# Optimization experiments

Measured on AMD Instinct MI355X. Metric: run time of the kernel, lower is better.

## Reference

```python
import jax, jax.numpy as jnp
import numpy as np

N = 1048576  # batch elements; each element is a 64-bit FP64 value stored as {0,1} float bits


def _xor(a, b):
    return a + b - 2.0 * a * b


def _mux(s, a, b):
    # s ? a : b  (spiking MUX gate)
    return s * a + (1.0 - s) * b


def _ripple_add(a, b, c0):
    """Bitwise ripple-carry add of little-endian bit vectors a,b [..., n] with carry-in c0 [...]."""
    def step(carry, ab):
        ai, bi = ab
        x = _xor(ai, bi)
        s = _xor(x, carry)
        c = ai * bi + carry * x - ai * bi * carry * x  # OR(a&b, c&(a^b))
        return c, s
    _, sums = jax.lax.scan(step, c0, (jnp.moveaxis(a, -1, 0), jnp.moveaxis(b, -1, 0)))
    return jnp.moveaxis(sums, 0, -1)


def setup_inputs() -> dict:
    key = jax.random.key(0)
    kx, kk = jax.random.split(key)
    x = jax.random.randint(kx, (N, 64), 0, 2).astype(jnp.float32)
    k = jax.random.randint(kk, (N, 64), 0, 2).astype(jnp.float32)
    return {"x": x, "k": k}


def reference(x, k):
    batch = x.shape[:-1]
    dt = x.dtype
    ones = jnp.ones(batch, dt)
    zeros = jnp.zeros(batch, dt)

    s_x = x[..., 0:1]
    e_x = x[..., 1:12]
    m_x = x[..., 12:64]
    s_k = k[..., 0:1]
    e_k = k[..., 1:12]
    m_k = k[..., 12:64]

    # shift = e_k - 1023 (little-endian, two's complement via add of NOT(1023)+1)
    e_k_le = e_k[..., ::-1]
    not_1023_le = jnp.broadcast_to(jnp.asarray([0.0] * 10 + [1.0], dt), batch + (11,))
    shift = _ripple_add(e_k_le, not_1023_le, ones)

    # barrel shifter: integer value of |k| = (1.mantissa) >> (15 - shift)  over 16 bits
    s_bar = 1.0 - shift[..., :4]  # bits of (15 - shift)
    val = jnp.concatenate([jnp.ones(batch + (1,), dt), m_k[..., :15]], axis=-1)
    current = val[..., ::-1]  # little-endian
    for layer in range(4):
        amt = 1 << layer
        shifted = jnp.concatenate([current[..., amt:], jnp.zeros(batch + (amt,), dt)], axis=-1)
        current = _mux(s_bar[..., layer:layer + 1], shifted, current)
    k_abs_le = current[..., :11]

    # negate via two's complement; select by sign of k
    neg_k = _ripple_add(1.0 - k_abs_le, jnp.zeros(batch + (11,), dt), ones)
    k_final = _mux(s_k, neg_k, k_abs_le)

    # e_new = e_x + k_final
    e_x_le = e_x[..., ::-1]
    e_new = _ripple_add(e_x_le, k_final, zeros)[..., ::-1]

    # k == 0 detection: OR-reduce bits 1..63 (OR(a,b)=1-(1-a)(1-b)), then NOT
    k_is_zero = jnp.prod(1.0 - k[..., 1:64], axis=-1, keepdims=True)

    result_scaled = jnp.concatenate([s_x, e_new, m_x], axis=-1)
    return _mux(k_is_zero, x, result_scaled)
```

## Files before the change

### kernel.cpp

```cpp
#include <hip/hip_runtime.h>


__global__ __launch_bounds__(256) void spike_fp64_scale_kernel(
    const float* __restrict__ x,
    const float* __restrict__ k,
    float* __restrict__ out,
    int nrows)
{
    const int gid  = blockIdx.x * blockDim.x + threadIdx.x;
    const int row  = gid >> 6;
    const int lane = threadIdx.x & 63;
    if (row >= nrows) return;

    const size_t base = (size_t)row * 64 + lane;
    const float xf = x[base];
    const float kf = k[base];

    const unsigned long long mx = __ballot(xf != 0.0f);
    const unsigned long long mk = __ballot(kf != 0.0f);
    const unsigned long long ux = __builtin_bitreverse64(mx);
    const unsigned long long uk = __builtin_bitreverse64(mk);

    const unsigned ek = (unsigned)(uk >> 52) & 0x7FFu;
    const unsigned sh = (ek + 1u) & 15u;

    const unsigned val16 = (1u << 15) | ((unsigned)(uk >> 37) & 0x7FFFu);

    const unsigned kabs = (val16 >> (15u - sh)) & 0x7FFu;

    const unsigned kfin = (uk >> 63) ? ((0u - kabs) & 0x7FFu) : kabs;

    const unsigned ex   = (unsigned)(ux >> 52) & 0x7FFu;
    const unsigned enew = (ex + kfin) & 0x7FFu;

    const bool kzero = (uk & 0x7FFFFFFFFFFFFFFFull) == 0ull;
    const unsigned long long uscaled =
        (ux & ~(0x7FFull << 52)) | ((unsigned long long)enew << 52);
    const unsigned long long uout = kzero ? ux : uscaled;

    out[base] = (float)((uout >> (63 - lane)) & 1ull);
}

extern "C" void kernel_launch(void* const* d_in, const int* in_sizes, int n_in,
                              void* d_out, int out_size, void* d_ws, size_t ws_size,
                              hipStream_t stream) {
    const float* x = (const float*)d_in[0];
    const float* k = (const float*)d_in[1];
    float* out = (float*)d_out;

    const int nrows = in_sizes[0] / 64;
    const int threads = 256;
    const int total_threads = nrows * 64;
    const int blocks = (total_threads + threads - 1) / threads;

    spike_fp64_scale_kernel<<<blocks, threads, 0, stream>>>(x, k, out, nrows);
}
```

Before: 582.9 us.

## Vectorize loads to float4 and pack rows via 16-lane shuffle OR reduction

Result: faster. 570.8 us (-2.1%).

```diff
diff --git a/kernel.cpp b/kernel.cpp
--- a/kernel.cpp
+++ b/kernel.cpp
@@ -1,57 +1,79 @@
 #include <hip/hip_runtime.h>
 
 
+__device__ __forceinline__ unsigned long long shfl_xor_u64(unsigned long long v, int m) {
+    unsigned lo = (unsigned)v;
+    unsigned hi = (unsigned)(v >> 32);
+    lo = (unsigned)__shfl_xor((int)lo, m, 64);
+    hi = (unsigned)__shfl_xor((int)hi, m, 64);
+    return ((unsigned long long)hi << 32) | lo;
+}
+
 __global__ __launch_bounds__(256) void spike_fp64_scale_kernel(
-    const float* __restrict__ x,
-    const float* __restrict__ k,
-    float* __restrict__ out,
+    const float4* __restrict__ x4,
+    const float4* __restrict__ k4,
+    float4* __restrict__ o4,
     int nrows)
 {
-    const int gid  = blockIdx.x * blockDim.x + threadIdx.x;
-    const int row  = gid >> 6;
+    const int wid  = (blockIdx.x * blockDim.x + threadIdx.x) >> 6;
     const int lane = threadIdx.x & 63;
+    const int g    = lane >> 4;
+    const int j    = lane & 15;
+    const int row  = wid * 4 + g;
     if (row >= nrows) return;
 
-    const size_t base = (size_t)row * 64 + lane;
-    const float xf = x[base];
-    const float kf = k[base];
+    const size_t idx = (size_t)row * 16 + j;
+    const float4 xv = x4[idx];
+    const float4 kv = k4[idx];
 
-    const unsigned long long mx = __ballot(xf != 0.0f);
-    const unsigned long long mk = __ballot(kf != 0.0f);
-    const unsigned long long ux = __builtin_bitreverse64(mx);
-    const unsigned long long uk = __builtin_bitreverse64(mk);
+    const unsigned nx = (xv.x != 0.0f ? 1u : 0u) | (xv.y != 0.0f ? 2u : 0u)
+                      | (xv.z != 0.0f ? 4u : 0u) | (xv.w != 0.0f ? 8u : 0u);
+    const unsigned nk = (kv.x != 0.0f ? 1u : 0u) | (kv.y != 0.0f ? 2u : 0u)
+                      | (kv.z != 0.0f ? 4u : 0u) | (kv.w != 0.0f ? 8u : 0u);
+
+    const unsigned long long REV4 = 0xF7B3D591E6A2C480ull;
+    const int sh = 60 - 4 * j;
+    unsigned long long ux = ((REV4 >> (nx * 4)) & 0xFull) << sh;
+    unsigned long long uk = ((REV4 >> (nk * 4)) & 0xFull) << sh;
+
+    #pragma unroll
+    for (int m = 1; m <= 8; m <<= 1) {
+        ux |= shfl_xor_u64(ux, m);
+        uk |= shfl_xor_u64(uk, m);
+    }
 
     const unsigned ek = (unsigned)(uk >> 52) & 0x7FFu;
-    const unsigned sh = (ek + 1u) & 15u;
-
+    const unsigned shv = (ek + 1u) & 15u;
     const unsigned val16 = (1u << 15) | ((unsigned)(uk >> 37) & 0x7FFFu);
-
-    const unsigned kabs = (val16 >> (15u - sh)) & 0x7FFu;
-
+    const unsigned kabs = (val16 >> (15u - shv)) & 0x7FFu;
     const unsigned kfin = (uk >> 63) ? ((0u - kabs) & 0x7FFu) : kabs;
-
     const unsigned ex   = (unsigned)(ux >> 52) & 0x7FFu;
     const unsigned enew = (ex + kfin) & 0x7FFu;
-
     const bool kzero = (uk & 0x7FFFFFFFFFFFFFFFull) == 0ull;
     const unsigned long long uscaled =
         (ux & ~(0x7FFull << 52)) | ((unsigned long long)enew << 52);
     const unsigned long long uout = kzero ? ux : uscaled;
 
-    out[base] = (float)((uout >> (63 - lane)) & 1ull);
+    const unsigned nout = (unsigned)((uout >> sh) & 0xFull);
+    float4 o;
+    o.x = (float)((nout >> 3) & 1u);
+    o.y = (float)((nout >> 2) & 1u);
+    o.z = (float)((nout >> 1) & 1u);
+    o.w = (float)( nout       & 1u);
+    o4[idx] = o;
 }
 
 extern "C" void kernel_launch(void* const* d_in, const int* in_sizes, int n_in,
                               void* d_out, int out_size, void* d_ws, size_t ws_size,
                               hipStream_t stream) {
-    const float* x = (const float*)d_in[0];
-    const float* k = (const float*)d_in[1];
-    float* out = (float*)d_out;
+    const float4* x4 = (const float4*)d_in[0];
+    const float4* k4 = (const float4*)d_in[1];
+    float4* o4 = (float4*)d_out;
 
     const int nrows = in_sizes[0] / 64;
+    const int total_threads = nrows * 16;
     const int threads = 256;
-    const int total_threads = nrows * 64;
     const int blocks = (total_threads + threads - 1) / threads;
 
-    spike_fp64_scale_kernel<<<blocks, threads, 0, stream>>>(x, k, out, nrows);
+    spike_fp64_scale_kernel<<<blocks, threads, 0, stream>>>(x4, k4, o4, nrows);
 }
```

## Vectorize row processing with 16-byte loads, grid-stride prefetch, nontemporal stores

Applied to the files above, without the earlier changes.

Result: slower. 602.2 us (+3.3%).

```diff
diff --git a/kernel.cpp b/kernel.cpp
--- a/kernel.cpp
+++ b/kernel.cpp
@@ -1,57 +1,99 @@
 #include <hip/hip_runtime.h>
 
 
+typedef unsigned int u32x4 __attribute__((ext_vector_type(4)));
+
 __global__ __launch_bounds__(256) void spike_fp64_scale_kernel(
-    const float* __restrict__ x,
-    const float* __restrict__ k,
-    float* __restrict__ out,
-    int nrows)
+    const u32x4* __restrict__ x4,
+    const u32x4* __restrict__ k4,
+    u32x4* __restrict__ o4,
+    int ntiles)
 {
-    const int gid  = blockIdx.x * blockDim.x + threadIdx.x;
-    const int row  = gid >> 6;
-    const int lane = threadIdx.x & 63;
-    if (row >= nrows) return;
+    const int nwaves = (int)((gridDim.x * blockDim.x) >> 6);
+    const int wid    = (int)((blockIdx.x * blockDim.x + threadIdx.x) >> 6);
+    const int lane   = (int)(threadIdx.x & 63);
+    const int g      = lane >> 4;
+    const int j      = lane & 15;
 
-    const size_t base = (size_t)row * 64 + lane;
-    const float xf = x[base];
-    const float kf = k[base];
+    if (wid >= ntiles) return;
 
-    const unsigned long long mx = __ballot(xf != 0.0f);
-    const unsigned long long mk = __ballot(kf != 0.0f);
-    const unsigned long long ux = __builtin_bitreverse64(mx);
-    const unsigned long long uk = __builtin_bitreverse64(mk);
+    size_t idx        = (size_t)wid * 64 + lane;
+    const size_t step = (size_t)nwaves * 64;
 
-    const unsigned ek = (unsigned)(uk >> 52) & 0x7FFu;
-    const unsigned sh = (ek + 1u) & 15u;
+    u32x4 xv = x4[idx];
+    u32x4 kv = k4[idx];
 
-    const unsigned val16 = (1u << 15) | ((unsigned)(uk >> 37) & 0x7FFFu);
+    int tile = wid;
+    for (;;) {
+        const int  nxt      = tile + nwaves;
+        const bool has_next = nxt < ntiles;
+        u32x4 xn, kn;
+        if (has_next) {
+            xn = x4[idx + step];
+            kn = k4[idx + step];
+        }
 
-    const unsigned kabs = (val16 >> (15u - sh)) & 0x7FFu;
+        const unsigned nx = ((xv[0] >> 23) & 1u) | ((xv[1] >> 22) & 2u)
+                          | ((xv[2] >> 21) & 4u) | ((xv[3] >> 20) & 8u);
+        const unsigned nk = ((kv[0] >> 23) & 1u) | ((kv[1] >> 22) & 2u)
+                          | ((kv[2] >> 21) & 4u) | ((kv[3] >> 20) & 8u);
 
-    const unsigned kfin = (uk >> 63) ? ((0u - kabs) & 0x7FFu) : kabs;
+        const unsigned sh4 = (unsigned)(j & 7) * 4u;
+        unsigned uxl = (j < 8) ? (nx << sh4) : 0u;
+        unsigned ukl = (j < 8) ? (nk << sh4) : 0u;
 
-    const unsigned ex   = (unsigned)(ux >> 52) & 0x7FFu;
-    const unsigned enew = (ex + kfin) & 0x7FFu;
+        const unsigned nkm = nk & ((j == 0) ? 0xEu : 0xFu);
+        const unsigned long long bal = __ballot(nkm != 0u);
+        const bool kany = ((unsigned)((bal >> (g * 16)) & 0xFFFFull)) != 0u;
 
-    const bool kzero = (uk & 0x7FFFFFFFFFFFFFFFull) == 0ull;
-    const unsigned long long uscaled =
-        (ux & ~(0x7FFull << 52)) | ((unsigned long long)enew << 52);
-    const unsigned long long uout = kzero ? ux : uscaled;
+        #pragma unroll
+        for (int m = 1; m <= 8; m <<= 1) {
+            uxl |= (unsigned)__shfl_xor((int)uxl, m, 64);
+            ukl |= (unsigned)__shfl_xor((int)ukl, m, 64);
+        }
 
-    out[base] = (float)((uout >> (63 - lane)) & 1ull);
+        const unsigned bk    = __builtin_bitreverse32(ukl);
+        const unsigned ek    = (bk >> 20) & 0x7FFu;
+        const unsigned val16 = 0x8000u | ((bk >> 5) & 0x7FFFu);
+        const unsigned shv   = (ek + 1u) & 15u;
+        const unsigned kabs  = (val16 >> (15u - shv)) & 0x7FFu;
+        const unsigned kfin  = (ukl & 1u) ? ((0u - kabs) & 0x7FFu) : kabs;
+        const unsigned ex    = (__builtin_bitreverse32(uxl) >> 20) & 0x7FFu;
+        const unsigned enew  = (ex + kfin) & 0x7FFu;
+
+        u32x4 o;
+        const int e0 = 4 * j;
+        #pragma unroll
+        for (int c = 0; c < 4; ++c) {
+            const int e = e0 + c;
+            const unsigned bit  = (enew >> (((unsigned)(11 - e)) & 31u)) & 1u;
+            const bool     repl = kany && (e >= 1) && (e <= 11);
+            o[c] = repl ? (bit ? 0x3F800000u : 0u) : xv[c];
+        }
+        __builtin_nontemporal_store(o, &o4[idx]);
+
+        if (!has_next) break;
+        tile = nxt;
+        idx += step;
+        xv = xn;
+        kv = kn;
+    }
 }
 
 extern "C" void kernel_launch(void* const* d_in, const int* in_sizes, int n_in,
                               void* d_out, int out_size, void* d_ws, size_t ws_size,
                               hipStream_t stream) {
-    const float* x = (const float*)d_in[0];
-    const float* k = (const float*)d_in[1];
-    float* out = (float*)d_out;
+    const u32x4* x4 = (const u32x4*)d_in[0];
+    const u32x4* k4 = (const u32x4*)d_in[1];
+    u32x4* o4 = (u32x4*)d_out;
 
-    const int nrows = in_sizes[0] / 64;
+    const int nrows  = in_sizes[0] / 64;
+    const int ntiles = nrows / 4;
+
     const int threads = 256;
-    const int total_threads = nrows * 64;
-    const int blocks = (total_threads + threads - 1) / threads;
+    int blocks = 2048;
+    const int max_blocks = (ntiles * 64 + threads - 1) / threads;
+    if (blocks > max_blocks) blocks = max_blocks;
 
-    spike_fp64_scale_kernel<<<blocks, threads, 0, stream>>>(x, k, out, nrows);
+    spike_fp64_scale_kernel<<<blocks, threads, 0, stream>>>(x4, k4, o4, ntiles);
 }
```
